# Performance work log

Hardware: AMD Instinct MI355X
Metric: run time of the kernel (lower is better)

## Reference

```python
import jax, jax.numpy as jnp
import numpy as np

B, S, D, H = 4, 1024, 1024, 16
DK = D // H


def setup_inputs() -> dict:
    key = jax.random.key(0)
    ks = jax.random.split(key, 14)
    scale = 1.0 / np.sqrt(D)
    inp = {
        "Qx": jax.random.normal(ks[0], (B, S, D), jnp.float32),
        "Kx": jax.random.normal(ks[1], (B, S, D), jnp.float32),
        "Vx": jax.random.normal(ks[2], (B, S, D), jnp.float32),
        "prob_phn": jax.random.uniform(ks[3], (B, S, S), jnp.float32),
        "mask": jax.random.randint(ks[4], (B, S, S), 0, 2, jnp.int32),
        "lambda_val": 1,
        "Wq": jax.random.normal(ks[5], (D, D), jnp.float32) * scale,
        "bq": jnp.zeros((D,), jnp.float32),
        "Wk": jax.random.normal(ks[6], (D, D), jnp.float32) * scale,
        "bk": jnp.zeros((D,), jnp.float32),
        "Wv": jax.random.normal(ks[7], (D, D), jnp.float32) * scale,
        "bv": jnp.zeros((D,), jnp.float32),
        "Wo": jax.random.normal(ks[8], (D, D), jnp.float32) * scale,
        "bo": jnp.zeros((D,), jnp.float32),
    }
    return inp


def _split_heads(x):
    # [B,S,D] -> [B,H,S,DK]
    b, s, _ = x.shape
    return x.reshape(b, s, H, DK).transpose(0, 2, 1, 3)


def reference(Qx, Kx, Vx, prob_phn, mask, lambda_val, Wq, bq, Wk, bk, Wv, bv, Wo, bo):
    q = _split_heads(Qx @ Wq.T + bq)
    k = _split_heads(Kx @ Wk.T + bk)
    v = _split_heads(Vx @ Wv.T + bv)
    scores = jnp.einsum("bhqd,bhkd->bhqk", q, k) / jnp.sqrt(jnp.float32(DK))
    if lambda_val > 0:
        # prob_phn: [B,S,S] -> transpose last two dims, broadcast over heads
        scores = scores - lambda_val * jnp.swapaxes(prob_phn, -2, -1)[:, None]
    scores = jnp.where(mask[:, None] == 0, jnp.float32(-1e9), scores)
    probs = jax.nn.softmax(scores, axis=-1)
    attn = jnp.einsum("bhqk,bhkd->bhqd", probs, v)
    out = attn.transpose(0, 2, 1, 3).reshape(Qx.shape[0], Qx.shape[1], D)
    out = out @ Wo.T + bo
    return (out, mask)
```

## Files before the change

kernel.cpp:

```cpp
#include <hip/hip_runtime.h>
#include <hip/hip_bf16.h>
#include <cstdint>
#include <cstddef>

#define BB 4
#define SS 1024
#define DD 1024
#define HH 16
#define DKK 64

typedef unsigned short u16;
typedef __bf16 bf16_t;
typedef __attribute__((ext_vector_type(8))) bf16_t bf16x8;
typedef __attribute__((ext_vector_type(4))) float floatx4;

#define LOG2E 1.4426950408889634f
#define QKSCALE 0.18033688011112042f

static __device__ inline u16 f2bf(float f) {
    union { float f; unsigned u; } v; v.f = f;
    unsigned r = v.u + 0x7fffu + ((v.u >> 16) & 1u);
    return (u16)(r >> 16);
}

static __device__ inline void load16_lds(const void* g, void* l) {
    __builtin_amdgcn_global_load_lds(
        (const __attribute__((address_space(1))) unsigned int*)g,
        (__attribute__((address_space(3))) unsigned int*)l,
        16, 0, 0);
}

static __device__ inline int swz64(int row, int c) { return row * 64 + ((c ^ (row & 7)) * 8); }
static __device__ inline int swz32(int row, int c) { return row * 32 + ((c ^ ((row >> 1) & 3)) * 8); }

static __device__ inline float lam_val(const int* p) {
    int v = *p;
    if (v >= -100000 && v <= 100000) return (float)v;
    union { int i; float f; } u; u.i = v; return u.f;
}

__global__ void prep_kernel(const float* __restrict__ Qx, const float* __restrict__ Kx,
                            const float* __restrict__ Vx,
                            const float* __restrict__ Wq, const float* __restrict__ Wk,
                            const float* __restrict__ Wv, const float* __restrict__ Wo,
                            const float* __restrict__ prob, const int* __restrict__ mask,
                            const int* __restrict__ lam_p,
                            u16* __restrict__ Xq, u16* __restrict__ Xk, u16* __restrict__ Xv,
                            u16* __restrict__ wq, u16* __restrict__ wk,
                            u16* __restrict__ wv, u16* __restrict__ wo,
                            u16* __restrict__ biasB, float* __restrict__ maskOut)
{
    __shared__ float tile[64][65];
    const int blk = blockIdx.x, tid = threadIdx.x;

    if (blk >= 1024) {
        const int cb = blk - 1024;
        const int base = cb * 1024;
        const float* src; u16* dst; int off0;
        if (base < 3145728) {
            int s = base >> 20;  off0 = base & 1048575;
            src = (s == 0) ? Qx : (s == 1) ? Kx : Vx;
            dst = (s == 0) ? Xq : (s == 1) ? Xk : Xv;
        } else {
            int v2 = base - 3145728;
            int s = v2 >> 18;  off0 = v2 & 262143;
            src = (s == 0) ? Wq : (s == 1) ? Wk : (s == 2) ? Wv : Wo;
            dst = (s == 0) ? wq : (s == 1) ? wk : (s == 2) ? wv : wo;
        }
        float4 f[4];
        #pragma unroll
        for (int r = 0; r < 4; ++r)
            f[r] = ((const float4*)src)[off0 + r * 256 + tid];
        #pragma unroll
        for (int r = 0; r < 4; ++r) {
            ushort4 o;
            o.x = f2bf(f[r].x); o.y = f2bf(f[r].y);
            o.z = f2bf(f[r].z); o.w = f2bf(f[r].w);
            ((ushort4*)dst)[off0 + r * 256 + tid] = o;
        }
        return;
    }

    const int b = blk >> 8;
    const int q0 = ((blk >> 4) & 15) * 64, k0 = (blk & 15) * 64;
    #pragma unroll
    for (int rr = 0; rr < 4; ++rr) {
        int unit = rr * 256 + tid;
        int kl = unit >> 4, qi = unit & 15;
        float4 p4 = *(const float4*)&prob[((size_t)(b * SS + k0 + kl)) * SS + q0 + qi * 4];
        tile[kl][qi * 4 + 0] = p4.x;
        tile[kl][qi * 4 + 1] = p4.y;
        tile[kl][qi * 4 + 2] = p4.z;
        tile[kl][qi * 4 + 3] = p4.w;
    }
    __syncthreads();
    const float lamc = lam_val(lam_p) * LOG2E;
    #pragma unroll
    for (int rr = 0; rr < 4; ++rr) {
        int pair = rr * 256 + tid;
        int q = pair >> 4, k4 = pair & 15;
        size_t oidx = ((size_t)(b * SS + q0 + q)) * SS + k0 + k4 * 4;
        int4 m4 = *(const int4*)&mask[oidx];
        float p0 = tile[k4 * 4 + 0][q];
        float p1 = tile[k4 * 4 + 1][q];
        float p2 = tile[k4 * 4 + 2][q];
        float p3 = tile[k4 * 4 + 3][q];
        ushort4 bb;
        bb.x = f2bf((m4.x == 0) ? -1.5e9f : -lamc * p0);
        bb.y = f2bf((m4.y == 0) ? -1.5e9f : -lamc * p1);
        bb.z = f2bf((m4.z == 0) ? -1.5e9f : -lamc * p2);
        bb.w = f2bf((m4.w == 0) ? -1.5e9f : -lamc * p3);
        *(ushort4*)&biasB[oidx] = bb;
        if (maskOut) {
            float4 mf = { (float)m4.x, (float)m4.y, (float)m4.z, (float)m4.w };
            *(float4*)&maskOut[oidx] = mf;
        }
    }
}

template <int MODE>
static __device__ inline void gemm_body(const u16* __restrict__ A, const u16* __restrict__ W,
                                        const float* __restrict__ bias,
                                        u16* __restrict__ Cb, float* __restrict__ Cf)
{
    constexpr int K = 1024, N = 1024;
    __shared__ __align__(16) u16 As[128 * 32];
    __shared__ __align__(16) u16 Bs[128 * 32];
    const int tid = threadIdx.x;
    const int wv = tid >> 6, ln = tid & 63, l15 = ln & 15, quad = ln >> 4;
    const int mBase = blockIdx.y * 128;
    const int nBase = blockIdx.x * 128;
    const int wm = (wv & 1) * 64, wn = (wv >> 1) * 64;

    const u16* Aptr[2]; const u16* Wptr[2];
    #pragma unroll
    for (int r = 0; r < 2; ++r) {
        int p = r * 256 + wv * 64 + ln;
        int row = p >> 2;
        int c = (p & 3) ^ ((row >> 1) & 3);
        Aptr[r] = A + (size_t)(mBase + row) * K + c * 8;
        Wptr[r] = W + (size_t)(nBase + row) * K + c * 8;
    }

    floatx4 acc[4][4] = {};

    for (int k0 = 0; k0 < K; k0 += 32) {
        __syncthreads();
        #pragma unroll
        for (int r = 0; r < 2; ++r) {
            load16_lds(Aptr[r] + k0, &As[(r * 256 + wv * 64) * 8]);
            load16_lds(Wptr[r] + k0, &Bs[(r * 256 + wv * 64) * 8]);
        }
        __syncthreads();
        bf16x8 af[4], bfr[4];
        #pragma unroll
        for (int i = 0; i < 4; ++i)
            af[i] = *(const bf16x8*)&As[swz32(wm + i * 16 + l15, quad)];
        #pragma unroll
        for (int j = 0; j < 4; ++j)
            bfr[j] = *(const bf16x8*)&Bs[swz32(wn + j * 16 + l15, quad)];
        #pragma unroll
        for (int i = 0; i < 4; ++i)
            #pragma unroll
            for (int j = 0; j < 4; ++j)
                acc[i][j] = __builtin_amdgcn_mfma_f32_16x16x32_bf16(af[i], bfr[j], acc[i][j], 0, 0, 0);
    }

    #pragma unroll
    for (int i = 0; i < 4; ++i) {
        #pragma unroll
        for (int j = 0; j < 4; ++j) {
            int col = nBase + wn + j * 16 + l15;
            float bcol = bias[col];
            if (MODE == 2) {
                int hh = col >> 6, dk = col & 63;
                int row0 = mBase + wm + i * 16 + quad * 4;
                int bb = row0 >> 10, s = row0 & 1023;
                ushort4 v4;
                v4.x = f2bf(acc[i][j][0] + bcol);
                v4.y = f2bf(acc[i][j][1] + bcol);
                v4.z = f2bf(acc[i][j][2] + bcol);
                v4.w = f2bf(acc[i][j][3] + bcol);
                *(ushort4*)&Cb[((size_t)((bb * HH + hh) * DKK) + dk) * SS + s] = v4;
            } else {
                #pragma unroll
                for (int r = 0; r < 4; ++r) {
                    int row = mBase + wm + i * 16 + quad * 4 + r;
                    float v = acc[i][j][r] + bcol;
                    if (MODE == 1) Cf[(size_t)row * N + col] = v;
                    else           Cb[(size_t)row * N + col] = f2bf(v);
                }
            }
        }
    }
}

__global__ __launch_bounds__(256) void gemm_qkv_kernel(
    const u16* __restrict__ Xq, const u16* __restrict__ Xk, const u16* __restrict__ Xv,
    const u16* __restrict__ Wq, const u16* __restrict__ Wk, const u16* __restrict__ Wv,
    const float* __restrict__ bq, const float* __restrict__ bk, const float* __restrict__ bv,
    u16* __restrict__ Cq, u16* __restrict__ Ck, u16* __restrict__ Vtout)
{
    const int z = blockIdx.z;
    if (z == 2) {
        gemm_body<2>(Xv, Wv, bv, Vtout, nullptr);
    } else {
        const u16* A = (z == 0) ? Xq : Xk;
        const u16* W = (z == 0) ? Wq : Wk;
        const float* bias = (z == 0) ? bq : bk;
        u16* C = (z == 0) ? Cq : Ck;
        gemm_body<0>(A, W, bias, C, nullptr);
    }
}

__global__ __launch_bounds__(256) void gemm_out_kernel(
    const u16* __restrict__ A, const u16* __restrict__ W,
    const float* __restrict__ bias, float* __restrict__ Cf)
{
    gemm_body<1>(A, W, bias, nullptr, Cf);
}

__global__ __launch_bounds__(256) void attn_kernel(
    const u16* __restrict__ Qf, const u16* __restrict__ Kf,
    const u16* __restrict__ Vt, const u16* __restrict__ biasB,
    u16* __restrict__ Attn)
{
    __shared__ __align__(16) u16 Qs[64 * 64];
    __shared__ __align__(16) u16 Ks[64 * 64];
    __shared__ __align__(16) u16 Vs[64 * 64];
    __shared__ __align__(16) u16 Ps[4][16 * 72];
    __shared__ float Rs[4][16];
    const int tid = threadIdx.x;
    const int wv = tid >> 6, ln = tid & 63, l15 = ln & 15, quad = ln >> 4;

    const int lin = blockIdx.x + 16 * blockIdx.y + 256 * blockIdx.z;
    const int sw  = (lin & 7) * 128 + (lin >> 3);
    const int qt = sw & 15, h = (sw >> 4) & 15, b = sw >> 8;
    const int q0 = qt * 64;

    int row64[2], col64[2];
    #pragma unroll
    for (int r = 0; r < 2; ++r) {
        int p = r * 256 + wv * 64 + ln;
        row64[r] = p >> 3;
        col64[r] = ((p & 7) ^ (row64[r] & 7)) * 8;
    }

    #pragma unroll
    for (int r = 0; r < 2; ++r)
        load16_lds(Qf + ((size_t)(b * SS + q0 + row64[r])) * DD + h * DKK + col64[r],
                   &Qs[(r * 256 + wv * 64) * 8]);
    __syncthreads();

    bf16x8 aq[2];
    #pragma unroll
    for (int t = 0; t < 2; ++t)
        aq[t] = *(const bf16x8*)&Qs[swz64(wv * 16 + l15, t * 4 + quad)];

    const size_t vt_head = ((size_t)(b * HH + h)) * DKK * SS;
    const u16* Kp[2]; const u16* Vp[2];
    #pragma unroll
    for (int r = 0; r < 2; ++r) {
        Kp[r] = Kf + ((size_t)(b * SS + row64[r])) * DD + h * DKK + col64[r];
        Vp[r] = Vt + vt_head + (size_t)row64[r] * SS + col64[r];
    }

    const u16* bp = biasB + ((size_t)(b * SS + q0 + wv * 16 + l15)) * SS + quad * 4;

    floatx4 o[4] = {};
    float rsum = 0.f;

    for (int kt = 0; kt < 16; ++kt) {
        const int kk0 = kt * 64;
        __syncthreads();
        #pragma unroll
        for (int r = 0; r < 2; ++r) {
            load16_lds(Kp[r] + (size_t)kk0 * DD, &Ks[(r * 256 + wv * 64) * 8]);
            load16_lds(Vp[r] + kk0, &Vs[(r * 256 + wv * 64) * 8]);
        }
        __syncthreads();

        uint2 braw[4];
        #pragma unroll
        for (int j = 0; j < 4; ++j)
            braw[j] = *(const uint2*)&bp[kk0 + j * 16];

        floatx4 sfr[4];
        #pragma unroll
        for (int j = 0; j < 4; ++j) {
            bf16x8 bk0 = *(const bf16x8*)&Ks[swz64(j * 16 + l15, quad)];
            bf16x8 bk1 = *(const bf16x8*)&Ks[swz64(j * 16 + l15, 4 + quad)];
            floatx4 s = {};
            s = __builtin_amdgcn_mfma_f32_16x16x32_bf16(bk0, aq[0], s, 0, 0, 0);
            sfr[j] = __builtin_amdgcn_mfma_f32_16x16x32_bf16(bk1, aq[1], s, 0, 0, 0);
        }

        #pragma unroll
        for (int j = 0; j < 4; ++j) {
            float b0 = __uint_as_float(braw[j].x << 16);
            float b1 = __uint_as_float(braw[j].x & 0xffff0000u);
            float b2 = __uint_as_float(braw[j].y << 16);
            float b3 = __uint_as_float(braw[j].y & 0xffff0000u);
            float p0 = __builtin_amdgcn_exp2f(fmaf(sfr[j][0], QKSCALE, b0));
            float p1 = __builtin_amdgcn_exp2f(fmaf(sfr[j][1], QKSCALE, b1));
            float p2 = __builtin_amdgcn_exp2f(fmaf(sfr[j][2], QKSCALE, b2));
            float p3 = __builtin_amdgcn_exp2f(fmaf(sfr[j][3], QKSCALE, b3));
            rsum += (p0 + p1) + (p2 + p3);
            uint2 pk;
            pk.x = (__float_as_uint(p0) >> 16) | (__float_as_uint(p1) & 0xffff0000u);
            pk.y = (__float_as_uint(p2) >> 16) | (__float_as_uint(p3) & 0xffff0000u);
            *(uint2*)&Ps[wv][l15 * 72 + j * 16 + quad * 4] = pk;
        }

        #pragma unroll
        for (int t = 0; t < 2; ++t) {
            bf16x8 ap = *(const bf16x8*)&Ps[wv][l15 * 72 + t * 32 + quad * 8];
            #pragma unroll
            for (int j = 0; j < 4; ++j) {
                bf16x8 bvv = *(const bf16x8*)&Vs[swz64(j * 16 + l15, t * 4 + quad)];
                o[j] = __builtin_amdgcn_mfma_f32_16x16x32_bf16(ap, bvv, o[j], 0, 0, 0);
            }
        }
    }

    rsum += __shfl_xor(rsum, 16);
    rsum += __shfl_xor(rsum, 32);
    if (ln < 16) Rs[wv][l15] = 1.0f / rsum;
    float4 rv = *(const float4*)&Rs[wv][quad * 4];

    #pragma unroll
    for (int j = 0; j < 4; ++j) {
        #pragma unroll
        for (int r = 0; r < 4; ++r) {
            int srow = q0 + wv * 16 + quad * 4 + r;
            int dk = j * 16 + l15;
            float ri = (r == 0) ? rv.x : (r == 1) ? rv.y : (r == 2) ? rv.z : rv.w;
            Attn[((size_t)(b * SS + srow)) * DD + h * DKK + dk] = f2bf(o[j][r] * ri);
        }
    }
}

extern "C" void kernel_launch(void* const* d_in, const int* in_sizes, int n_in,
                              void* d_out, int out_size, void* d_ws, size_t ws_size,
                              hipStream_t stream)
{
    const float* Qx  = (const float*)d_in[0];
    const float* Kx  = (const float*)d_in[1];
    const float* Vx  = (const float*)d_in[2];
    const float* prob = (const float*)d_in[3];
    const int*   mask = (const int*)d_in[4];
    const int*   lam  = (const int*)d_in[5];
    const float* Wq  = (const float*)d_in[6];
    const float* bq  = (const float*)d_in[7];
    const float* Wk  = (const float*)d_in[8];
    const float* bk  = (const float*)d_in[9];
    const float* Wv  = (const float*)d_in[10];
    const float* bv  = (const float*)d_in[11];
    const float* Wo  = (const float*)d_in[12];
    const float* bo  = (const float*)d_in[13];

    char* ws = (char*)d_ws;
    const size_t MB = 1024 * 1024;
    u16*   Xq     = (u16*)(ws + 0 * MB);
    u16*   Xk     = (u16*)(ws + 8 * MB);
    u16*   Xv     = (u16*)(ws + 16 * MB);
    u16*   wq     = (u16*)(ws + 24 * MB);
    u16*   wk     = (u16*)(ws + 26 * MB);
    u16*   wvp    = (u16*)(ws + 28 * MB);
    u16*   wo     = (u16*)(ws + 30 * MB);
    u16*   q_flat = (u16*)(ws + 32 * MB);
    u16*   k_flat = (u16*)(ws + 40 * MB);
    u16*   vt     = (u16*)(ws + 56 * MB);
    u16*   biasB  = (u16*)(ws + 64 * MB);
    u16*   attn   = (u16*)(ws + 80 * MB);

    float* maskOut = (out_size >= 2 * BB * SS * DD) ? (float*)d_out + (size_t)BB * SS * DD
                                                    : nullptr;

    prep_kernel<<<5120, 256, 0, stream>>>(Qx, Kx, Vx, Wq, Wk, Wv, Wo, prob, mask, lam,
                                          Xq, Xk, Xv, wq, wk, wvp, wo, biasB, maskOut);
    gemm_qkv_kernel<<<dim3(8, 32, 3), 256, 0, stream>>>(Xq, Xk, Xv, wq, wk, wvp,
                                                        bq, bk, bv, q_flat, k_flat, vt);
    attn_kernel<<<dim3(16, 16, 4), 256, 0, stream>>>(q_flat, k_flat, vt, biasB, attn);
    gemm_out_kernel<<<dim3(8, 32, 1), 256, 0, stream>>>(attn, wo, bo, (float*)d_out);
}
```

Baseline: 262.2 us.

## Store attention bias in a per-tile fragment layout and vectorize output writes

The prep kernel now stages the bias tile in shared memory and writes it out in a layout ordered by key tile, fragment and q row. This lets each lane of the attention kernel load its bias fragment with contiguous, coalesced 8-byte reads instead of strided row reads. The PV MFMA operands are swapped so each lane holds four consecutive head-dim outputs for a single q row. That removes the shared-memory reciprocal exchange and allows packed ushort4 stores to Attn. It costs an extra shared-memory pass and barrier in the prep kernel.

```diff
diff --git a/kernel.cpp b/kernel.cpp
--- a/kernel.cpp
+++ b/kernel.cpp
@@ -48,9 +48,10 @@
                             u16* __restrict__ Xq, u16* __restrict__ Xk, u16* __restrict__ Xv,
                             u16* __restrict__ wq, u16* __restrict__ wk,
                             u16* __restrict__ wv, u16* __restrict__ wo,
-                            u16* __restrict__ biasB, float* __restrict__ maskOut)
+                            u16* __restrict__ biasT, float* __restrict__ maskOut)
 {
     __shared__ float tile[64][65];
+    __shared__ u16 btile[64][68];
     const int blk = blockIdx.x, tid = threadIdx.x;
 
     if (blk >= 1024) {
@@ -83,6 +84,7 @@
 
     const int b = blk >> 8;
     const int q0 = ((blk >> 4) & 15) * 64, k0 = (blk & 15) * 64;
+    const int kt = blk & 15;
     #pragma unroll
     for (int rr = 0; rr < 4; ++rr) {
         int unit = rr * 256 + tid;
@@ -99,8 +101,8 @@
     for (int rr = 0; rr < 4; ++rr) {
         int pair = rr * 256 + tid;
         int q = pair >> 4, k4 = pair & 15;
-        size_t oidx = ((size_t)(b * SS + q0 + q)) * SS + k0 + k4 * 4;
-        int4 m4 = *(const int4*)&mask[oidx];
+        size_t midx = ((size_t)(b * SS + q0 + q)) * SS + k0 + k4 * 4;
+        int4 m4 = *(const int4*)&mask[midx];
         float p0 = tile[k4 * 4 + 0][q];
         float p1 = tile[k4 * 4 + 1][q];
         float p2 = tile[k4 * 4 + 2][q];
@@ -110,11 +112,20 @@
         bb.y = f2bf((m4.y == 0) ? -1.5e9f : -lamc * p1);
         bb.z = f2bf((m4.z == 0) ? -1.5e9f : -lamc * p2);
         bb.w = f2bf((m4.w == 0) ? -1.5e9f : -lamc * p3);
-        *(ushort4*)&biasB[oidx] = bb;
+        *(ushort4*)&btile[q][k4 * 4] = bb;
         if (maskOut) {
             float4 mf = { (float)m4.x, (float)m4.y, (float)m4.z, (float)m4.w };
-            *(float4*)&maskOut[oidx] = mf;
-        }
+            *(float4*)&maskOut[midx] = mf;
+        }
+    }
+    __syncthreads();
+    u16* bT = biasT + (size_t)(b * 16 + kt) * 65536;
+    #pragma unroll
+    for (int rr = 0; rr < 4; ++rr) {
+        int idx = rr * 256 + tid;
+        int j = idx >> 8, quad = (idx >> 6) & 3, ql = idx & 63;
+        ushort4 v = *(const ushort4*)&btile[ql][j * 16 + quad * 4];
+        *(ushort4*)&bT[(size_t)((j * 4 + quad) * 1024 + q0 + ql) * 4] = v;
     }
 }
 
@@ -222,14 +233,13 @@
 
 __global__ __launch_bounds__(256) void attn_kernel(
     const u16* __restrict__ Qf, const u16* __restrict__ Kf,
-    const u16* __restrict__ Vt, const u16* __restrict__ biasB,
+    const u16* __restrict__ Vt, const u16* __restrict__ biasT,
     u16* __restrict__ Attn)
 {
     __shared__ __align__(16) u16 Qs[64 * 64];
     __shared__ __align__(16) u16 Ks[64 * 64];
     __shared__ __align__(16) u16 Vs[64 * 64];
     __shared__ __align__(16) u16 Ps[4][16 * 72];
-    __shared__ float Rs[4][16];
     const int tid = threadIdx.x;
     const int wv = tid >> 6, ln = tid & 63, l15 = ln & 15, quad = ln >> 4;
 
@@ -265,7 +275,8 @@
         Vp[r] = Vt + vt_head + (size_t)row64[r] * SS + col64[r];
     }
 
-    const u16* bp = biasB + ((size_t)(b * SS + q0 + wv * 16 + l15)) * SS + quad * 4;
+    const int qq = q0 + wv * 16 + l15;
+    const u16* bpT = biasT + (size_t)b * 1048576 + (size_t)quad * 4096 + (size_t)qq * 4;
 
     floatx4 o[4] = {};
     float rsum = 0.f;
@@ -283,7 +294,7 @@
         uint2 braw[4];
         #pragma unroll
         for (int j = 0; j < 4; ++j)
-            braw[j] = *(const uint2*)&bp[kk0 + j * 16];
+            braw[j] = *(const uint2*)&bpT[(size_t)kt * 65536 + j * 16384];
 
         floatx4 sfr[4];
         #pragma unroll
@@ -318,25 +329,24 @@
             #pragma unroll
             for (int j = 0; j < 4; ++j) {
                 bf16x8 bvv = *(const bf16x8*)&Vs[swz64(j * 16 + l15, t * 4 + quad)];
-                o[j] = __builtin_amdgcn_mfma_f32_16x16x32_bf16(ap, bvv, o[j], 0, 0, 0);
+                o[j] = __builtin_amdgcn_mfma_f32_16x16x32_bf16(bvv, ap, o[j], 0, 0, 0);
             }
         }
     }
 
     rsum += __shfl_xor(rsum, 16);
     rsum += __shfl_xor(rsum, 32);
-    if (ln < 16) Rs[wv][l15] = 1.0f / rsum;
-    float4 rv = *(const float4*)&Rs[wv][quad * 4];
-
+    const float ri = 1.0f / rsum;
+
+    u16* outp = Attn + ((size_t)(b * SS + qq)) * DD + h * DKK + quad * 4;
     #pragma unroll
     for (int j = 0; j < 4; ++j) {
-        #pragma unroll
-        for (int r = 0; r < 4; ++r) {
-            int srow = q0 + wv * 16 + quad * 4 + r;
-            int dk = j * 16 + l15;
-            float ri = (r == 0) ? rv.x : (r == 1) ? rv.y : (r == 2) ? rv.z : rv.w;
-            Attn[((size_t)(b * SS + srow)) * DD + h * DKK + dk] = f2bf(o[j][r] * ri);
-        }
+        ushort4 v4;
+        v4.x = f2bf(o[j][0] * ri);
+        v4.y = f2bf(o[j][1] * ri);
+        v4.z = f2bf(o[j][2] * ri);
+        v4.w = f2bf(o[j][3] * ri);
+        *(ushort4*)&outp[j * 16] = v4;
     }
 }
 
@@ -371,16 +381,16 @@
     u16*   q_flat = (u16*)(ws + 32 * MB);
     u16*   k_flat = (u16*)(ws + 40 * MB);
     u16*   vt     = (u16*)(ws + 56 * MB);
-    u16*   biasB  = (u16*)(ws + 64 * MB);
+    u16*   biasT  = (u16*)(ws + 64 * MB);
     u16*   attn   = (u16*)(ws + 80 * MB);
 
     float* maskOut = (out_size >= 2 * BB * SS * DD) ? (float*)d_out + (size_t)BB * SS * DD
                                                     : nullptr;
 
     prep_kernel<<<5120, 256, 0, stream>>>(Qx, Kx, Vx, Wq, Wk, Wv, Wo, prob, mask, lam,
-                                          Xq, Xk, Xv, wq, wk, wvp, wo, biasB, maskOut);
+                                          Xq, Xk, Xv, wq, wk, wvp, wo, biasT, maskOut);
     gemm_qkv_kernel<<<dim3(8, 32, 3), 256, 0, stream>>>(Xq, Xk, Xv, wq, wk, wvp,
                                                         bq, bk, bv, q_flat, k_flat, vt);
-    attn_kernel<<<dim3(16, 16, 4), 256, 0, stream>>>(q_flat, k_flat, vt, biasB, attn);
+    attn_kernel<<<dim3(16, 16, 4), 256, 0, stream>>>(q_flat, k_flat, vt, biasT, attn);
     gemm_out_kernel<<<dim3(8, 32, 1), 256, 0, stream>>>(attn, wo, bo, (float*)d_out);
 }
```

Result: no change. 258.8 us (-1.3%).
